# Kernel tuning notes

Measured on AMD Instinct MI355X. Metric: run time of the kernel, lower is better.

Reference implementation:

```python
import jax, jax.numpy as jnp
import numpy as np

N, E, IN, HID, OUT = 100000, 1600000, 128, 128, 64


def setup_inputs() -> dict:
    key = jax.random.key(0)
    k1, k2, k3, k4 = jax.random.split(key, 4)
    x = jax.random.normal(k1, (N, IN), dtype=jnp.float32)
    edge_index = jax.random.randint(k2, (2, E), 0, N, dtype=jnp.int64)
    W1 = jax.random.normal(k3, (IN, HID), dtype=jnp.float32) * (1.0 / np.sqrt(IN))
    b1 = jnp.zeros((HID,), dtype=jnp.float32)
    W2 = jax.random.normal(k4, (HID, OUT), dtype=jnp.float32) * (1.0 / np.sqrt(HID))
    b2 = jnp.zeros((OUT,), dtype=jnp.float32)
    return {"x": x, "edge_index": edge_index, "W1": W1, "b1": b1, "W2": W2, "b2": b2}


def _gcn_conv(x, src, dst, norm, W, b):
    # linear transform first (PyG order when reducing feature dim), then SpMM
    h = x @ W                                   # [N, F_out]
    msg = h[src] * norm[:, None]                # [E+N, F_out] gathered messages
    out = jax.ops.segment_sum(msg, dst, num_segments=x.shape[0])
    return out + b


def _norm_coeffs(edge_index, num_nodes, dtype):
    # add self-loops and compute symmetric normalization deg^-1/2[src]*deg^-1/2[dst]
    loop = jnp.arange(num_nodes, dtype=edge_index.dtype)
    src = jnp.concatenate([edge_index[0], loop])
    dst = jnp.concatenate([edge_index[1], loop])
    deg = jax.ops.segment_sum(jnp.ones_like(dst, dtype=dtype), dst, num_segments=num_nodes)
    dinv = jnp.where(deg > 0, jax.lax.rsqrt(jnp.maximum(deg, 1.0)), 0.0)
    norm = dinv[src] * dinv[dst]
    return src, dst, norm


def reference(x, edge_index, W1, b1, W2, b2):
    # eval-mode forward: dropout is identity
    src, dst, norm = _norm_coeffs(edge_index, x.shape[0], x.dtype)
    h = jax.nn.relu(_gcn_conv(x, src, dst, norm, W1, b1))
    out = _gcn_conv(h, src, dst, norm, W2, b2)
    return out
```

## Files before the change

kernel.cpp:

```cpp
#include <hip/hip_runtime.h>
#include <hip/hip_bf16.h>

#define DEVINL __device__ __forceinline__

DEVINL int clampidx(int v, int n) { return ((unsigned)v < (unsigned)n) ? v : 0; }
DEVINL float bflo(unsigned int u) { return __uint_as_float(u << 16); }
DEVINL float bfhi(unsigned int u) { return __uint_as_float(u & 0xffff0000u); }
DEVINL unsigned int f2bf(float f) {
    unsigned int u = __float_as_uint(f);
    u += 0x7fffu + ((u >> 16) & 1u);
    return u >> 16;
}

__global__ __launch_bounds__(256) void k_bktcount(const int* __restrict__ ei,
                                                  int* __restrict__ bktCnt, int E, int n) {
    __shared__ int hist[1024];
    for (int i = threadIdx.x; i < 1024; i += 256) hist[i] = 0;
    __syncthreads();
    const int base = blockIdx.x * 4096;
#pragma unroll
    for (int j = 0; j < 16; ++j) {
        int i = base + j * 256 + threadIdx.x;
        if (i < E) atomicAdd(&hist[clampidx(ei[(size_t)E + i], n) >> 7], 1);
    }
    __syncthreads();
    for (int b = threadIdx.x; b < 1024; b += 256) {
        int c = hist[b];
        if (c) atomicAdd(&bktCnt[b], c);
    }
}

__global__ __launch_bounds__(256) void k_bktscan(const int* __restrict__ bktCnt,
                                                 int* __restrict__ bktBase,
                                                 int* __restrict__ bktCur, int NB) {
    __shared__ int sh[256];
    int carry = 0;
    for (int c0 = 0; c0 < NB; c0 += 256) {
        const int i = c0 + threadIdx.x;
        const int v = (i < NB) ? bktCnt[i] : 0;
        sh[threadIdx.x] = v;
        __syncthreads();
        for (int off = 1; off < 256; off <<= 1) {
            int t = (threadIdx.x >= off) ? sh[threadIdx.x - off] : 0;
            __syncthreads();
            sh[threadIdx.x] += t;
            __syncthreads();
        }
        if (i < NB) {
            const int excl = carry + sh[threadIdx.x] - v;
            bktBase[i] = excl;
            bktCur[i] = excl;
        }
        const int tot = sh[255];
        __syncthreads();
        carry += tot;
    }
    if (threadIdx.x == 0) bktBase[NB] = carry;
}

__global__ __launch_bounds__(256) void k_bktscatter(const int* __restrict__ ei,
                                                    int* __restrict__ bktCur,
                                                    unsigned int* __restrict__ packed,
                                                    int E, int n) {
    __shared__ unsigned int sPack[4096];
    __shared__ unsigned short sBkt[4096];
    __shared__ int sHist[1024], sStart[1024], sLoc[1024];
    for (int i = threadIdx.x; i < 1024; i += 256) {
        sHist[i] = 0;
        sLoc[i] = 0;
    }
    __syncthreads();
    const int base = blockIdx.x * 4096;
#pragma unroll
    for (int j = 0; j < 16; ++j) {
        const int k = j * 256 + threadIdx.x;
        const int i = base + k;
        if (i < E) {
            const int s = clampidx(ei[i], n);
            const int d = clampidx(ei[(size_t)E + i], n);
            const int b = d >> 7;
            sPack[k] = ((unsigned)(d & 127) << 25) | (unsigned)s;
            sBkt[k] = (unsigned short)b;
            atomicAdd(&sHist[b], 1);
        }
    }
    __syncthreads();
    for (int b = threadIdx.x; b < 1024; b += 256) {
        const int c = sHist[b];
        sStart[b] = c ? atomicAdd(&bktCur[b], c) : 0;
    }
    __syncthreads();
#pragma unroll
    for (int j = 0; j < 16; ++j) {
        const int k = j * 256 + threadIdx.x;
        const int i = base + k;
        if (i < E) {
            const int b = sBkt[k];
            const int pos = sStart[b] + atomicAdd(&sLoc[b], 1);
            packed[pos] = sPack[k];
        }
    }
}

__global__ __launch_bounds__(256) void k_bktfill(const unsigned int* __restrict__ packed,
                                                 const int* __restrict__ bktBase,
                                                 int* __restrict__ p, float* __restrict__ dinv,
                                                 int* __restrict__ srcs, int n) {
    constexpr int CAP = 8192;
    __shared__ unsigned int sPack[CAP];
    __shared__ int sSrc[CAP];
    __shared__ int deg[128], incl[128], cur[128];
    const int bkt = blockIdx.x;
    const int e0 = bktBase[bkt], e1 = bktBase[bkt + 1];
    const int cnt = e1 - e0;
    const int tid = threadIdx.x;
    if (tid < 128) deg[tid] = 0;
    __syncthreads();
    for (int i = tid; i < cnt; i += 256) {
        const unsigned int u = packed[e0 + i];
        if (i < CAP) sPack[i] = u;
        atomicAdd(&deg[u >> 25], 1);
    }
    __syncthreads();
    if (tid < 128) incl[tid] = deg[tid];
    __syncthreads();
    for (int off = 1; off < 128; off <<= 1) {
        const int v = (tid < 128 && tid >= off) ? incl[tid - off] : 0;
        __syncthreads();
        if (tid < 128) incl[tid] += v;
        __syncthreads();
    }
    const int node0 = bkt << 7;
    if (tid < 128) {
        cur[tid] = incl[tid] - deg[tid];
        const int node = node0 + tid;
        if (node < n) {
            p[node] = e0 + incl[tid];
            dinv[node] = rsqrtf((float)deg[tid] + 1.0f);
        }
    }
    __syncthreads();
    for (int i = tid; i < cnt; i += 256) {
        const unsigned int u = (i < CAP) ? sPack[i] : packed[e0 + i];
        const int dl = (int)(u >> 25);
        const int s = (int)(u & 0x1FFFFFFu);
        const int pos = atomicAdd(&cur[dl], 1);
        if (pos < CAP) sSrc[pos] = s;
        else srcs[e0 + pos] = s;
    }
    __syncthreads();
    const int lim = cnt < CAP ? cnt : CAP;
    for (int i = tid; i < lim; i += 256) srcs[e0 + i] = sSrc[i];
}

template <int BCOLS, bool IN_BF16>
__global__ __launch_bounds__(256) void k_gemm_rt(const void* __restrict__ Xv,
                                                 const float* __restrict__ W,
                                                 unsigned int* __restrict__ Y, int ystrideU,
                                                 int n) {
    constexpr int KC = 32;
    constexpr int CG = BCOLS / 8;
    constexpr int RG = 256 / CG;
    constexpr int BROWS = RG * 4;
    constexpr int P = BROWS + 4;
    __shared__ float Ws[KC * BCOLS];
    __shared__ float xs[KC * P];

    const int tid = threadIdx.x;
    const int row0 = blockIdx.x * BROWS;
    const int ct = tid % CG;
    const int rt = tid / CG;

    float acc[4][8];
#pragma unroll
    for (int i = 0; i < 4; ++i)
#pragma unroll
        for (int j = 0; j < 8; ++j) acc[i][j] = 0.0f;

    for (int k0 = 0; k0 < 128; k0 += KC) {
        __syncthreads();
        for (int idx = tid * 4; idx < KC * BCOLS; idx += 1024)
            *(float4*)&Ws[idx] = *(const float4*)&W[(size_t)k0 * BCOLS + idx];
        if (IN_BF16) {
            const int row = tid >> 1, q = tid & 1;
            const int grow = row0 + row;
            const unsigned int* src =
                (const unsigned int*)Xv + (size_t)grow * 64 + (k0 >> 1) + q * 8;
            uint4 u0 = make_uint4(0, 0, 0, 0), u1 = make_uint4(0, 0, 0, 0);
            if (grow < n) {
                u0 = *(const uint4*)src;
                u1 = *(const uint4*)(src + 4);
            }
            const int kb = q * 16;
            float* xp = &xs[row];
            xp[(kb + 0) * P] = bflo(u0.x); xp[(kb + 1) * P] = bfhi(u0.x);
            xp[(kb + 2) * P] = bflo(u0.y); xp[(kb + 3) * P] = bfhi(u0.y);
            xp[(kb + 4) * P] = bflo(u0.z); xp[(kb + 5) * P] = bfhi(u0.z);
            xp[(kb + 6) * P] = bflo(u0.w); xp[(kb + 7) * P] = bfhi(u0.w);
            xp[(kb + 8) * P] = bflo(u1.x); xp[(kb + 9) * P] = bfhi(u1.x);
            xp[(kb + 10) * P] = bflo(u1.y); xp[(kb + 11) * P] = bfhi(u1.y);
            xp[(kb + 12) * P] = bflo(u1.z); xp[(kb + 13) * P] = bfhi(u1.z);
            xp[(kb + 14) * P] = bflo(u1.w); xp[(kb + 15) * P] = bfhi(u1.w);
        } else {
            const int row = tid >> 2, q = tid & 3;
            const int grow = row0 + row;
            const float* src = (const float*)Xv + (size_t)grow * 128 + k0 + q * 8;
            float4 v0 = make_float4(0, 0, 0, 0), v1 = make_float4(0, 0, 0, 0);
            if (grow < n) {
                v0 = *(const float4*)src;
                v1 = *(const float4*)(src + 4);
            }
            const int kb = q * 8;
            float* xp = &xs[row];
            xp[(kb + 0) * P] = v0.x; xp[(kb + 1) * P] = v0.y;
            xp[(kb + 2) * P] = v0.z; xp[(kb + 3) * P] = v0.w;
            xp[(kb + 4) * P] = v1.x; xp[(kb + 5) * P] = v1.y;
            xp[(kb + 6) * P] = v1.z; xp[(kb + 7) * P] = v1.w;
        }
        __syncthreads();

#pragma unroll 8
        for (int k = 0; k < KC; ++k) {
            const float4 xv = *(const float4*)&xs[k * P + rt * 4];
            const float4 wA = *(const float4*)&Ws[k * BCOLS + ct * 8];
            const float4 wB = *(const float4*)&Ws[k * BCOLS + ct * 8 + 4];
            const float xr[4] = {xv.x, xv.y, xv.z, xv.w};
#pragma unroll
            for (int i = 0; i < 4; ++i) {
                acc[i][0] = fmaf(xr[i], wA.x, acc[i][0]);
                acc[i][1] = fmaf(xr[i], wA.y, acc[i][1]);
                acc[i][2] = fmaf(xr[i], wA.z, acc[i][2]);
                acc[i][3] = fmaf(xr[i], wA.w, acc[i][3]);
                acc[i][4] = fmaf(xr[i], wB.x, acc[i][4]);
                acc[i][5] = fmaf(xr[i], wB.y, acc[i][5]);
                acc[i][6] = fmaf(xr[i], wB.z, acc[i][6]);
                acc[i][7] = fmaf(xr[i], wB.w, acc[i][7]);
            }
        }
    }

#pragma unroll
    for (int i = 0; i < 4; ++i) {
        const int row = row0 + rt * 4 + i;
        if (row < n) {
            uint4 o;
            o.x = f2bf(acc[i][0]) | (f2bf(acc[i][1]) << 16);
            o.y = f2bf(acc[i][2]) | (f2bf(acc[i][3]) << 16);
            o.z = f2bf(acc[i][4]) | (f2bf(acc[i][5]) << 16);
            o.w = f2bf(acc[i][6]) | (f2bf(acc[i][7]) << 16);
            *(uint4*)&Y[(size_t)row * ystrideU + ct * 4] = o;
        }
    }
}

__global__ __launch_bounds__(256) void k_gather128(const unsigned int* __restrict__ XW,
                                                   const int* __restrict__ p,
                                                   const int* __restrict__ srcs,
                                                   const float* __restrict__ dinv,
                                                   const float* __restrict__ b1,
                                                   unsigned int* __restrict__ H1b, int n) {
    const int node = __builtin_amdgcn_readfirstlane(blockIdx.x * 4 + (threadIdx.x >> 6));
    if (node >= n) return;
    const int t = threadIdx.x & 63;
    const int start = (node == 0) ? 0 : p[node - 1];
    const int end = p[node];
    const float din = dinv[node];
    const unsigned int us = XW[(size_t)node * 64 + t];
    float a0 = bflo(us) * din, a1 = bfhi(us) * din;

    int c = start;
    for (; c + 8 <= end; c += 8) {
        int s[8];
#pragma unroll
        for (int k = 0; k < 8; ++k) s[k] = __builtin_amdgcn_readfirstlane(srcs[c + k]);
        float w[8];
        unsigned int u[8];
#pragma unroll
        for (int k = 0; k < 8; ++k) {
            w[k] = dinv[s[k]];
            u[k] = XW[((unsigned)s[k] << 6) + t];
        }
#pragma unroll
        for (int k = 0; k < 8; ++k) {
            a0 = fmaf(bflo(u[k]), w[k], a0);
            a1 = fmaf(bfhi(u[k]), w[k], a1);
        }
    }
    for (; c < end; ++c) {
        const int s = __builtin_amdgcn_readfirstlane(srcs[c]);
        const float w = dinv[s];
        const unsigned int u = XW[((unsigned)s << 6) + t];
        a0 = fmaf(bflo(u), w, a0);
        a1 = fmaf(bfhi(u), w, a1);
    }
    const float r0 = fmaxf(fmaf(a0, din, b1[2 * t]), 0.0f);
    const float r1 = fmaxf(fmaf(a1, din, b1[2 * t + 1]), 0.0f);
    H1b[(size_t)node * 64 + t] = f2bf(r0) | (f2bf(r1) << 16);
}

__global__ __launch_bounds__(256) void k_gather64(const unsigned short* __restrict__ h2,
                                                  const int* __restrict__ p,
                                                  const int* __restrict__ srcs,
                                                  const float* __restrict__ dinv,
                                                  const float* __restrict__ b2,
                                                  float* __restrict__ out, int n) {
    const int node = __builtin_amdgcn_readfirstlane(blockIdx.x * 4 + (threadIdx.x >> 6));
    if (node >= n) return;
    const int t = threadIdx.x & 63;
    const int start = (node == 0) ? 0 : p[node - 1];
    const int end = p[node];
    const float din = dinv[node];
    float acc = bflo(h2[(size_t)node * 64 + t]) * din;

    int c = start;
    for (; c + 8 <= end; c += 8) {
        int s[8];
#pragma unroll
        for (int k = 0; k < 8; ++k) s[k] = __builtin_amdgcn_readfirstlane(srcs[c + k]);
        float w[8], v[8];
#pragma unroll
        for (int k = 0; k < 8; ++k) {
            w[k] = dinv[s[k]];
            v[k] = bflo(h2[((unsigned)s[k] << 6) + t]);
        }
#pragma unroll
        for (int k = 0; k < 8; ++k) acc = fmaf(v[k], w[k], acc);
    }
    for (; c < end; ++c) {
        const int s = __builtin_amdgcn_readfirstlane(srcs[c]);
        const float w = dinv[s];
        acc = fmaf(bflo(h2[((unsigned)s << 6) + t]), w, acc);
    }
    out[(size_t)node * 64 + t] = fmaf(acc, din, b2[t]);
}

extern "C" void kernel_launch(void* const* d_in, const int* in_sizes, int n_in,
                              void* d_out, int out_size, void* d_ws, size_t ws_size,
                              hipStream_t stream) {
    const float* x  = (const float*)d_in[0];
    const int* ei   = (const int*)d_in[1];
    const float* W1 = (const float*)d_in[2];
    const float* b1 = (const float*)d_in[3];
    const float* W2 = (const float*)d_in[4];
    const float* b2 = (const float*)d_in[5];

    const int n = in_sizes[0] / 128;
    const int E = in_sizes[1] / 2;
    const int NB = (n + 127) >> 7;

    auto al = [](size_t b) { return (b + 255) & ~(size_t)255; };
    const size_t off_p    = 0;
    const size_t off_dinv = off_p + al((size_t)n * 4);
    const size_t off_srcs = off_dinv + al((size_t)n * 4);
    const size_t off_XW   = off_srcs + al((size_t)E * 4);
    const size_t off_H1b  = off_XW + al((size_t)n * 64 * 4);
    const size_t need     = off_H1b + (size_t)n * 64 * 4;
    const size_t off_pk   = off_H1b;
    const size_t off_bc   = off_pk + al((size_t)E * 4);
    const size_t off_bb   = off_bc + al(1024 * 4);
    const size_t off_bu   = off_bb + al(1025 * 4);

    if (ws_size < need || NB > 1024) {
        hipMemsetAsync(d_out, 0, (size_t)out_size * 4, stream);
        return;
    }

    int*          p    = (int*)((char*)d_ws + off_p);
    float*        dinv = (float*)((char*)d_ws + off_dinv);
    int*          srcs = (int*)((char*)d_ws + off_srcs);
    unsigned int* XW   = (unsigned int*)((char*)d_ws + off_XW);
    unsigned int* H1b  = (unsigned int*)((char*)d_ws + off_H1b);
    unsigned int* pk   = (unsigned int*)((char*)d_ws + off_pk);
    int*          bCnt = (int*)((char*)d_ws + off_bc);
    int*          bBase= (int*)((char*)d_ws + off_bb);
    int*          bCur = (int*)((char*)d_ws + off_bu);
    float*        out  = (float*)d_out;

    const int gEdge = (E + 4095) / 4096;
    const int gG    = (n + 3) / 4;

    hipMemsetAsync(bCnt, 0, 1024 * 4, stream);
    k_bktcount<<<gEdge, 256, 0, stream>>>(ei, bCnt, E, n);
    k_bktscan<<<1, 256, 0, stream>>>(bCnt, bBase, bCur, NB);
    k_bktscatter<<<gEdge, 256, 0, stream>>>(ei, bCur, pk, E, n);
    k_bktfill<<<NB, 256, 0, stream>>>(pk, bBase, p, dinv, srcs, n);

    k_gemm_rt<128, false><<<(n + 63) / 64, 256, 0, stream>>>(x, W1, XW, 64, n);

    k_gather128<<<gG, 256, 0, stream>>>(XW, p, srcs, dinv, b1, H1b, n);

    k_gemm_rt<64, true><<<(n + 127) / 128, 256, 0, stream>>>(H1b, W2, XW, 32, n);

    k_gather64<<<gG, 256, 0, stream>>>((const unsigned short*)XW, p, srcs, dinv, b2, out, n);
}
```

Measured before the change: 357.3 us.

## Split layer-1 gather across column halves and edge parity per wavefront

The 128-feature gather kernel now launches twice as many blocks. Each wavefront handles one 64-column half of a node's row. Within a wave, the two 32-lane halves process even and odd edges separately, and their partial sums are combined with a cross-lane shuffle. This doubles the number of wavefronts in flight and halves the serial edge loop per wave, trading redundant index and dinv loads and smaller 128-byte row segments per load for more memory-level parallelism.

```diff
diff --git a/kernel.cpp b/kernel.cpp
--- a/kernel.cpp
+++ b/kernel.cpp
@@ -259,43 +259,67 @@
                                                    const float* __restrict__ dinv,
                                                    const float* __restrict__ b1,
                                                    unsigned int* __restrict__ H1b, int n) {
-    const int node = __builtin_amdgcn_readfirstlane(blockIdx.x * 4 + (threadIdx.x >> 6));
+    const int half = blockIdx.x & 1;
+    const int node =
+        __builtin_amdgcn_readfirstlane((blockIdx.x >> 1) * 4 + (threadIdx.x >> 6));
     if (node >= n) return;
-    const int t = threadIdx.x & 63;
+    const int tl = threadIdx.x & 31;
+    const int hi = (threadIdx.x >> 5) & 1;
     const int start = (node == 0) ? 0 : p[node - 1];
     const int end = p[node];
     const float din = dinv[node];
-    const unsigned int us = XW[(size_t)node * 64 + t];
-    float a0 = bflo(us) * din, a1 = bfhi(us) * din;
-
+    const unsigned int* XWh = XW + (half << 5);
+
+    float a0 = 0.0f, a1 = 0.0f;
     int c = start;
     for (; c + 8 <= end; c += 8) {
         int s[8];
 #pragma unroll
         for (int k = 0; k < 8; ++k) s[k] = __builtin_amdgcn_readfirstlane(srcs[c + k]);
         float w[8];
-        unsigned int u[8];
-#pragma unroll
-        for (int k = 0; k < 8; ++k) {
-            w[k] = dinv[s[k]];
-            u[k] = XW[((unsigned)s[k] << 6) + t];
-        }
-#pragma unroll
-        for (int k = 0; k < 8; ++k) {
-            a0 = fmaf(bflo(u[k]), w[k], a0);
-            a1 = fmaf(bfhi(u[k]), w[k], a1);
-        }
-    }
-    for (; c < end; ++c) {
-        const int s = __builtin_amdgcn_readfirstlane(srcs[c]);
-        const float w = dinv[s];
-        const unsigned int u = XW[((unsigned)s << 6) + t];
-        a0 = fmaf(bflo(u), w, a0);
-        a1 = fmaf(bfhi(u), w, a1);
-    }
-    const float r0 = fmaxf(fmaf(a0, din, b1[2 * t]), 0.0f);
-    const float r1 = fmaxf(fmaf(a1, din, b1[2 * t + 1]), 0.0f);
-    H1b[(size_t)node * 64 + t] = f2bf(r0) | (f2bf(r1) << 16);
+#pragma unroll
+        for (int k = 0; k < 8; ++k) w[k] = dinv[s[k]];
+        unsigned int u[4];
+#pragma unroll
+        for (int q = 0; q < 4; ++q) {
+            const int sk = hi ? s[2 * q + 1] : s[2 * q];
+            u[q] = XWh[((size_t)sk << 6) + tl];
+        }
+#pragma unroll
+        for (int q = 0; q < 4; ++q) {
+            const float wk = hi ? w[2 * q + 1] : w[2 * q];
+            a0 = fmaf(bflo(u[q]), wk, a0);
+            a1 = fmaf(bfhi(u[q]), wk, a1);
+        }
+    }
+    for (; c + 2 <= end; c += 2) {
+        const int s0 = __builtin_amdgcn_readfirstlane(srcs[c]);
+        const int s1 = __builtin_amdgcn_readfirstlane(srcs[c + 1]);
+        const float w0 = dinv[s0], w1 = dinv[s1];
+        const int sk = hi ? s1 : s0;
+        const float wk = hi ? w1 : w0;
+        const unsigned int u = XWh[((size_t)sk << 6) + tl];
+        a0 = fmaf(bflo(u), wk, a0);
+        a1 = fmaf(bfhi(u), wk, a1);
+    }
+    if (c < end) {
+        const int s0 = __builtin_amdgcn_readfirstlane(srcs[c]);
+        const float wk = hi ? 0.0f : dinv[s0];
+        const unsigned int u = XWh[((size_t)s0 << 6) + tl];
+        a0 = fmaf(bflo(u), wk, a0);
+        a1 = fmaf(bfhi(u), wk, a1);
+    }
+    a0 += __shfl_xor(a0, 32);
+    a1 += __shfl_xor(a1, 32);
+
+    const unsigned int us = XW[((size_t)node << 6) + (half << 5) + tl];
+    a0 = fmaf(bflo(us), din, a0);
+    a1 = fmaf(bfhi(us), din, a1);
+
+    const int j = (half << 5) + tl;
+    const float r0 = fmaxf(fmaf(a0, din, b1[2 * j]), 0.0f);
+    const float r1 = fmaxf(fmaf(a1, din, b1[2 * j + 1]), 0.0f);
+    if (hi == 0) H1b[((size_t)node << 6) + j] = f2bf(r0) | (f2bf(r1) << 16);
 }
 
 __global__ __launch_bounds__(256) void k_gather64(const unsigned short* __restrict__ h2,
@@ -378,6 +402,7 @@
 
     const int gEdge = (E + 4095) / 4096;
     const int gG    = (n + 3) / 4;
+    const int gG2   = gG * 2;
 
     hipMemsetAsync(bCnt, 0, 1024 * 4, stream);
     k_bktcount<<<gEdge, 256, 0, stream>>>(ei, bCnt, E, n);
@@ -387,7 +412,7 @@
 
     k_gemm_rt<128, false><<<(n + 63) / 64, 256, 0, stream>>>(x, W1, XW, 64, n);
 
-    k_gather128<<<gG, 256, 0, stream>>>(XW, p, srcs, dinv, b1, H1b, n);
+    k_gather128<<<gG2, 256, 0, stream>>>(XW, p, srcs, dinv, b1, H1b, n);
 
     k_gemm_rt<64, true><<<(n + 127) / 128, 256, 0, stream>>>(H1b, W2, XW, 32, n);
 
```

Measured after the change: 749.7 us. 2.1x slower.

## Merge bucket-count into first GEMM launch and widen gather unroll to 16

Applied to the files above, without the earlier changes.

The edge bucket histogram kernel and the first x@W1 GEMM are combined into one launch. The first blocks do the histogram and the remaining blocks do the GEMM, so the two independent stages overlap and one launch is removed. The gather kernels now issue 16 independent neighbor loads per iteration instead of 8, with a 4-wide tail loop, to increase memory-level parallelism. The cost is higher register pressure in the gathers and a shared-memory footprint set by the larger GEMM tile for every block, including the histogram blocks.

```diff
diff --git a/kernel.cpp b/kernel.cpp
--- a/kernel.cpp
+++ b/kernel.cpp
@@ -10,24 +10,6 @@
     unsigned int u = __float_as_uint(f);
     u += 0x7fffu + ((u >> 16) & 1u);
     return u >> 16;
-}
-
-__global__ __launch_bounds__(256) void k_bktcount(const int* __restrict__ ei,
-                                                  int* __restrict__ bktCnt, int E, int n) {
-    __shared__ int hist[1024];
-    for (int i = threadIdx.x; i < 1024; i += 256) hist[i] = 0;
-    __syncthreads();
-    const int base = blockIdx.x * 4096;
-#pragma unroll
-    for (int j = 0; j < 16; ++j) {
-        int i = base + j * 256 + threadIdx.x;
-        if (i < E) atomicAdd(&hist[clampidx(ei[(size_t)E + i], n) >> 7], 1);
-    }
-    __syncthreads();
-    for (int b = threadIdx.x; b < 1024; b += 256) {
-        int c = hist[b];
-        if (c) atomicAdd(&bktCnt[b], c);
-    }
 }
 
 __global__ __launch_bounds__(256) void k_bktscan(const int* __restrict__ bktCnt,
@@ -154,20 +136,17 @@
 }
 
 template <int BCOLS, bool IN_BF16>
-__global__ __launch_bounds__(256) void k_gemm_rt(const void* __restrict__ Xv,
-                                                 const float* __restrict__ W,
-                                                 unsigned int* __restrict__ Y, int ystrideU,
-                                                 int n) {
+DEVINL void gemm_body(const void* __restrict__ Xv, const float* __restrict__ W,
+                      unsigned int* __restrict__ Y, int ystrideU, int n, int blk,
+                      float* Ws, float* xs) {
     constexpr int KC = 32;
     constexpr int CG = BCOLS / 8;
     constexpr int RG = 256 / CG;
     constexpr int BROWS = RG * 4;
     constexpr int P = BROWS + 4;
-    __shared__ float Ws[KC * BCOLS];
-    __shared__ float xs[KC * P];
 
     const int tid = threadIdx.x;
-    const int row0 = blockIdx.x * BROWS;
+    const int row0 = blk * BROWS;
     const int ct = tid % CG;
     const int rt = tid / CG;
 
@@ -253,6 +232,43 @@
     }
 }
 
+__global__ __launch_bounds__(256) void k_gemm64(const void* __restrict__ Xv,
+                                                const float* __restrict__ W,
+                                                unsigned int* __restrict__ Y, int ystrideU,
+                                                int n) {
+    __shared__ float Ws[32 * 64];
+    __shared__ float xs[32 * 132];
+    gemm_body<64, true>(Xv, W, Y, ystrideU, n, blockIdx.x, Ws, xs);
+}
+
+__global__ __launch_bounds__(256) void k_gemm128_count(const void* __restrict__ Xv,
+                                                       const float* __restrict__ W,
+                                                       unsigned int* __restrict__ Y, int n,
+                                                       const int* __restrict__ ei,
+                                                       int* __restrict__ bktCnt, int E,
+                                                       int nCnt) {
+    __shared__ float Ws[32 * 128];
+    __shared__ float xs[32 * 68];
+    if ((int)blockIdx.x < nCnt) {
+        int* hist = (int*)Ws;
+        for (int i = threadIdx.x; i < 1024; i += 256) hist[i] = 0;
+        __syncthreads();
+        const int base = blockIdx.x * 4096;
+#pragma unroll
+        for (int j = 0; j < 16; ++j) {
+            int i = base + j * 256 + threadIdx.x;
+            if (i < E) atomicAdd(&hist[clampidx(ei[(size_t)E + i], n) >> 7], 1);
+        }
+        __syncthreads();
+        for (int b = threadIdx.x; b < 1024; b += 256) {
+            int c = hist[b];
+            if (c) atomicAdd(&bktCnt[b], c);
+        }
+    } else {
+        gemm_body<128, false>(Xv, W, Y, 64, n, (int)blockIdx.x - nCnt, Ws, xs);
+    }
+}
+
 __global__ __launch_bounds__(256) void k_gather128(const unsigned int* __restrict__ XW,
                                                    const int* __restrict__ p,
                                                    const int* __restrict__ srcs,
@@ -269,19 +285,36 @@
     float a0 = bflo(us) * din, a1 = bfhi(us) * din;
 
     int c = start;
-    for (; c + 8 <= end; c += 8) {
-        int s[8];
-#pragma unroll
-        for (int k = 0; k < 8; ++k) s[k] = __builtin_amdgcn_readfirstlane(srcs[c + k]);
-        float w[8];
-        unsigned int u[8];
-#pragma unroll
-        for (int k = 0; k < 8; ++k) {
+    for (; c + 16 <= end; c += 16) {
+        int s[16];
+#pragma unroll
+        for (int k = 0; k < 16; ++k) s[k] = __builtin_amdgcn_readfirstlane(srcs[c + k]);
+        float w[16];
+        unsigned int u[16];
+#pragma unroll
+        for (int k = 0; k < 16; ++k) {
             w[k] = dinv[s[k]];
             u[k] = XW[((unsigned)s[k] << 6) + t];
         }
 #pragma unroll
-        for (int k = 0; k < 8; ++k) {
+        for (int k = 0; k < 16; ++k) {
+            a0 = fmaf(bflo(u[k]), w[k], a0);
+            a1 = fmaf(bfhi(u[k]), w[k], a1);
+        }
+    }
+    for (; c + 4 <= end; c += 4) {
+        int s[4];
+#pragma unroll
+        for (int k = 0; k < 4; ++k) s[k] = __builtin_amdgcn_readfirstlane(srcs[c + k]);
+        float w[4];
+        unsigned int u[4];
+#pragma unroll
+        for (int k = 0; k < 4; ++k) {
+            w[k] = dinv[s[k]];
+            u[k] = XW[((unsigned)s[k] << 6) + t];
+        }
+#pragma unroll
+        for (int k = 0; k < 4; ++k) {
             a0 = fmaf(bflo(u[k]), w[k], a0);
             a1 = fmaf(bfhi(u[k]), w[k], a1);
         }
@@ -313,18 +346,31 @@
     float acc = bflo(h2[(size_t)node * 64 + t]) * din;
 
     int c = start;
-    for (; c + 8 <= end; c += 8) {
-        int s[8];
-#pragma unroll
-        for (int k = 0; k < 8; ++k) s[k] = __builtin_amdgcn_readfirstlane(srcs[c + k]);
-        float w[8], v[8];
-#pragma unroll
-        for (int k = 0; k < 8; ++k) {
+    for (; c + 16 <= end; c += 16) {
+        int s[16];
+#pragma unroll
+        for (int k = 0; k < 16; ++k) s[k] = __builtin_amdgcn_readfirstlane(srcs[c + k]);
+        float w[16], v[16];
+#pragma unroll
+        for (int k = 0; k < 16; ++k) {
             w[k] = dinv[s[k]];
             v[k] = bflo(h2[((unsigned)s[k] << 6) + t]);
         }
 #pragma unroll
-        for (int k = 0; k < 8; ++k) acc = fmaf(v[k], w[k], acc);
+        for (int k = 0; k < 16; ++k) acc = fmaf(v[k], w[k], acc);
+    }
+    for (; c + 4 <= end; c += 4) {
+        int s[4];
+#pragma unroll
+        for (int k = 0; k < 4; ++k) s[k] = __builtin_amdgcn_readfirstlane(srcs[c + k]);
+        float w[4], v[4];
+#pragma unroll
+        for (int k = 0; k < 4; ++k) {
+            w[k] = dinv[s[k]];
+            v[k] = bflo(h2[((unsigned)s[k] << 6) + t]);
+        }
+#pragma unroll
+        for (int k = 0; k < 4; ++k) acc = fmaf(v[k], w[k], acc);
     }
     for (; c < end; ++c) {
         const int s = __builtin_amdgcn_readfirstlane(srcs[c]);
@@ -377,19 +423,19 @@
     float*        out  = (float*)d_out;
 
     const int gEdge = (E + 4095) / 4096;
+    const int gGemm = (n + 63) / 64;
     const int gG    = (n + 3) / 4;
 
     hipMemsetAsync(bCnt, 0, 1024 * 4, stream);
-    k_bktcount<<<gEdge, 256, 0, stream>>>(ei, bCnt, E, n);
+    k_gemm128_count<<<gEdge + gGemm, 256, 0, stream>>>(x, W1, XW, n, ei, bCnt, E, gEdge);
+
     k_bktscan<<<1, 256, 0, stream>>>(bCnt, bBase, bCur, NB);
     k_bktscatter<<<gEdge, 256, 0, stream>>>(ei, bCur, pk, E, n);
     k_bktfill<<<NB, 256, 0, stream>>>(pk, bBase, p, dinv, srcs, n);
 
-    k_gemm_rt<128, false><<<(n + 63) / 64, 256, 0, stream>>>(x, W1, XW, 64, n);
-
     k_gather128<<<gG, 256, 0, stream>>>(XW, p, srcs, dinv, b1, H1b, n);
 
-    k_gemm_rt<64, true><<<(n + 127) / 128, 256, 0, stream>>>(H1b, W2, XW, 32, n);
+    k_gemm64<<<(n + 127) / 128, 256, 0, stream>>>(H1b, W2, XW, 32, n);
 
     k_gather64<<<gG, 256, 0, stream>>>((const unsigned short*)XW, p, srcs, dinv, b2, out, n);
 }
```

New measurement: 351.0 us. No clear change (-1.8%).
